# Performance work log

Measured on AMD Instinct MI355X. Metric: run time of the kernel, lower is better.

## Reference

```python
import jax, jax.numpy as jnp
import numpy as np

N = 100000   # nodes
E = 1600000  # edges (avg degree 16)
DIN = 128
DH = 64


def setup_inputs() -> dict:
    key = jax.random.key(0)
    ks = jax.random.split(key, 6)
    x = jax.random.normal(ks[0], (N, DIN), dtype=jnp.float32)
    edge_index = jax.random.randint(ks[1], (2, E), 0, N, dtype=jnp.int32)
    W1 = jax.random.normal(ks[2], (DIN, DH), dtype=jnp.float32) * (1.0 / np.sqrt(DIN))
    b1 = jnp.zeros((DH,), dtype=jnp.float32)
    W2 = jax.random.normal(ks[3], (DH, DH), dtype=jnp.float32) * (1.0 / np.sqrt(DH))
    b2 = jnp.zeros((DH,), dtype=jnp.float32)
    alpha = jnp.full((DH,), 0.25, dtype=jnp.float32)  # PReLU per-channel slope (torch default 0.25)
    return {"x": x, "edge_index": edge_index, "W1": W1, "b1": b1, "W2": W2, "b2": b2, "alpha": alpha}


def _gcn_layer(h, src, dst, norm, W, b):
    # GCNConv: linear transform, then normalized scatter-add aggregation, then bias
    h = h @ W                                  # [N, dout]
    msg = h[src] * norm[:, None]               # [E+N, dout] gathered + scaled messages
    agg = jax.ops.segment_sum(msg, dst, num_segments=N)
    return agg + b


def reference(x, edge_index, W1, b1, W2, b2, alpha):
    src0, dst0 = edge_index[0], edge_index[1]
    # GCNConv default: add self-loops, symmetric normalization deg^{-1/2} A deg^{-1/2}
    loops = jnp.arange(N, dtype=src0.dtype)
    src = jnp.concatenate([src0, loops])
    dst = jnp.concatenate([dst0, loops])
    ones = jnp.ones(src.shape[0], dtype=x.dtype)
    deg = jax.ops.segment_sum(ones, dst, num_segments=N)
    dinv = jnp.where(deg > 0, jax.lax.rsqrt(deg), 0.0)
    norm = dinv[src] * dinv[dst]               # [E+N]

    prelu = lambda z: jnp.where(z >= 0, z, alpha * z)  # shared per-channel PReLU
    z = prelu(_gcn_layer(x, src, dst, norm, W1, b1))
    z = prelu(_gcn_layer(z, src, dst, norm, W2, b2))
    return z
```

## Files before the change

kernel.cpp:

```cpp
#include <hip/hip_runtime.h>
#include <hip/hip_bf16.h>

#define NN 100000
#define NE 1600000
#define NBUCK 391
#define CAP 5120
#define CHUNK 2048
#define PBLOCKS 782
#define MMBLOCKS 1563

typedef __attribute__((ext_vector_type(8))) short short8;
typedef __attribute__((ext_vector_type(4))) float f32x4;

static __device__ __forceinline__ unsigned short f2bf(float f) {
    unsigned u = __float_as_uint(f);
    unsigned r = (u + 0x7fffu + ((u >> 16) & 1u)) >> 16;
    return (unsigned short)r;
}
static __device__ __forceinline__ float bf_lo(unsigned u) {
    return __uint_as_float(u << 16);
}
static __device__ __forceinline__ float bf_hi(unsigned u) {
    return __uint_as_float(u & 0xffff0000u);
}
static __device__ __forceinline__ void acc8(float* acc, uint4 v, float nm) {
    acc[0] += bf_lo(v.x) * nm; acc[1] += bf_hi(v.x) * nm;
    acc[2] += bf_lo(v.y) * nm; acc[3] += bf_hi(v.y) * nm;
    acc[4] += bf_lo(v.z) * nm; acc[5] += bf_hi(v.z) * nm;
    acc[6] += bf_lo(v.w) * nm; acc[7] += bf_hi(v.w) * nm;
}

__global__ __launch_bounds__(256) void k_fat(const int* __restrict__ ei,
                                             int* __restrict__ bcur,
                                             unsigned* __restrict__ ebuf,
                                             const float* __restrict__ x,
                                             const float* __restrict__ W1,
                                             unsigned short* __restrict__ hout) {
    __shared__ __attribute__((aligned(16))) unsigned char smem[17408];
    int tid = threadIdx.x;
    if (blockIdx.x < PBLOCKS) {
        int* lh = (int*)smem;
        int* lbase = lh + NBUCK;
        int e0 = blockIdx.x * CHUNK;
        for (int i = tid; i < NBUCK; i += 256) lh[i] = 0;
        __syncthreads();
        #pragma unroll
        for (int k = 0; k < CHUNK; k += 256) {
            int e = e0 + k + tid;
            if (e < NE) atomicAdd(&lh[ei[NE + e] >> 8], 1);
        }
        __syncthreads();
        for (int i = tid; i < NBUCK; i += 256) {
            int c = lh[i];
            lbase[i] = c ? atomicAdd(&bcur[i], c) : 0;
            lh[i] = 0;
        }
        __syncthreads();
        #pragma unroll
        for (int k = 0; k < CHUNK; k += 256) {
            int e = e0 + k + tid;
            if (e < NE) {
                int d = ei[NE + e];
                int s = ei[e];
                int b = d >> 8;
                int r = atomicAdd(&lh[b], 1);
                int pos = lbase[b] + r;
                if (pos < CAP)
                    ebuf[(long)b * CAP + pos] = ((unsigned)s << 8) | (unsigned)(d & 255);
            }
        }
    } else {
        constexpr int K = 128, KP = K + 8;
        unsigned short* Wt = (unsigned short*)smem;
        for (int idx = tid; idx < K * 64; idx += 256) {
            int k = idx >> 6, n = idx & 63;
            Wt[n * KP + k] = f2bf(W1[idx]);
        }
        __syncthreads();
        int wave = tid >> 6, lane = tid & 63;
        int m = lane & 15, q = lane >> 4;
        int n0 = (blockIdx.x - PBLOCKS) * 64 + wave * 16;
        f32x4 acc[4] = {{0.f,0.f,0.f,0.f},{0.f,0.f,0.f,0.f},{0.f,0.f,0.f,0.f},{0.f,0.f,0.f,0.f}};
        int row = n0 + m;
        int rowc = row < NN ? row : NN - 1;
        const float* xr = x + (long)rowc * K;
        #pragma unroll
        for (int kk = 0; kk < K / 32; ++kk) {
            const float4* p = (const float4*)(xr + kk * 32 + q * 8);
            float4 v0 = p[0], v1 = p[1];
            float xv[8] = {v0.x, v0.y, v0.z, v0.w, v1.x, v1.y, v1.z, v1.w};
            short8 afrag;
            #pragma unroll
            for (int i2 = 0; i2 < 8; ++i2) afrag[i2] = (short)f2bf(xv[i2]);
            #pragma unroll
            for (int nt = 0; nt < 4; ++nt) {
                const short8* bp = (const short8*)&Wt[(nt * 16 + m) * KP + kk * 32 + q * 8];
                acc[nt] = __builtin_amdgcn_mfma_f32_16x16x32_bf16(afrag, *bp, acc[nt], 0, 0, 0);
            }
        }
        #pragma unroll
        for (int reg = 0; reg < 4; ++reg) {
            int node = n0 + q * 4 + reg;
            if (node < NN) {
                #pragma unroll
                for (int nt = 0; nt < 4; ++nt)
                    hout[(long)node * 64 + nt * 16 + m] = f2bf(acc[nt][reg]);
            }
        }
    }
}

__global__ __launch_bounds__(256) void k_build(const int* __restrict__ bcur,
                                               const unsigned* __restrict__ ebuf,
                                               unsigned* __restrict__ rowinfo,
                                               float* __restrict__ dinv,
                                               int* __restrict__ esrc) {
    __shared__ int cnt[256];
    __shared__ int wsum[4];
    int tid = threadIdx.x;
    int base = blockIdx.x * CAP;
    int nedge = bcur[blockIdx.x];
    if (nedge > CAP) nedge = CAP;
    cnt[tid] = 0;
    __syncthreads();
    for (int j = tid; j < nedge; j += 256)
        atomicAdd(&cnt[ebuf[base + j] & 255u], 1);
    __syncthreads();
    int v = cnt[tid];
    int lane = tid & 63;
    int incl = v;
    #pragma unroll
    for (int off = 1; off < 64; off <<= 1) {
        int t = __shfl_up(incl, off, 64);
        if (lane >= off) incl += t;
    }
    if (lane == 63) wsum[tid >> 6] = incl;
    __syncthreads();
    if (tid == 0) {
        int a = 0;
        #pragma unroll
        for (int w = 0; w < 4; ++w) { int t = wsum[w]; wsum[w] = a; a += t; }
    }
    __syncthreads();
    int ex = incl - v + wsum[tid >> 6];
    int node = blockIdx.x * 256 + tid;
    if (node < NN) {
        rowinfo[node] = ((unsigned)(base + ex) << 11) | (unsigned)v;
        dinv[node] = rsqrtf((float)(v + 1));
    }
    cnt[tid] = base + ex;
    __syncthreads();
    for (int j = tid; j < nedge; j += 256) {
        unsigned p = ebuf[base + j];
        int pos = atomicAdd(&cnt[p & 255u], 1);
        esrc[pos] = (int)(p >> 8);
    }
}

__global__ __launch_bounds__(256) void k_mm64(const unsigned short* __restrict__ in_,
                                              const float* __restrict__ W,
                                              unsigned short* __restrict__ hout) {
    constexpr int K = 64, KP = K + 8;
    __shared__ unsigned short Wt[64 * KP];
    int tid = threadIdx.x;
    for (int idx = tid; idx < K * 64; idx += 256) {
        int k = idx >> 6, n = idx & 63;
        Wt[n * KP + k] = f2bf(W[idx]);
    }
    __syncthreads();
    int wave = tid >> 6, lane = tid & 63;
    int m = lane & 15, q = lane >> 4;
    int n0 = blockIdx.x * 64 + wave * 16;
    f32x4 acc[4] = {{0.f,0.f,0.f,0.f},{0.f,0.f,0.f,0.f},{0.f,0.f,0.f,0.f},{0.f,0.f,0.f,0.f}};
    int row = n0 + m;
    int rowc = row < NN ? row : NN - 1;
    const unsigned short* xr = in_ + (long)rowc * K;
    #pragma unroll
    for (int kk = 0; kk < K / 32; ++kk) {
        short8 afrag = *(const short8*)(xr + kk * 32 + q * 8);
        #pragma unroll
        for (int nt = 0; nt < 4; ++nt) {
            const short8* bp = (const short8*)&Wt[(nt * 16 + m) * KP + kk * 32 + q * 8];
            acc[nt] = __builtin_amdgcn_mfma_f32_16x16x32_bf16(afrag, *bp, acc[nt], 0, 0, 0);
        }
    }
    #pragma unroll
    for (int reg = 0; reg < 4; ++reg) {
        int node = n0 + q * 4 + reg;
        if (node < NN) {
            #pragma unroll
            for (int nt = 0; nt < 4; ++nt)
                hout[(long)node * 64 + nt * 16 + m] = f2bf(acc[nt][reg]);
        }
    }
}

template <bool OUT_BF16>
__global__ __launch_bounds__(256) void k_agg(const unsigned* __restrict__ rowinfo,
                                             const int* __restrict__ esrc,
                                             const unsigned short* __restrict__ h,
                                             const float* __restrict__ dinv,
                                             const float* __restrict__ bias,
                                             const float* __restrict__ alpha,
                                             void* __restrict__ out_) {
    int sl = threadIdx.x & 7;
    int node = blockIdx.x * 32 + (threadIdx.x >> 3);
    if (node >= NN) return;
    unsigned u = rowinfo[node];
    int start = (int)(u >> 11);
    int cnt = (int)(u & 2047u);
    float dn = dinv[node];
    const unsigned short* hc = h + sl * 8;

    float acc[8];
    {
        uint4 hw = *(const uint4*)(hc + (long)node * 64);
        float d2 = dn * dn;
        acc[0] = bf_lo(hw.x) * d2; acc[1] = bf_hi(hw.x) * d2;
        acc[2] = bf_lo(hw.y) * d2; acc[3] = bf_hi(hw.y) * d2;
        acc[4] = bf_lo(hw.z) * d2; acc[5] = bf_hi(hw.z) * d2;
        acc[6] = bf_lo(hw.w) * d2; acc[7] = bf_hi(hw.w) * d2;
    }

    int i = 0;
    for (; i + 8 <= cnt; i += 8) {
        int s0 = esrc[start + i];
        int s1 = esrc[start + i + 1];
        int s2 = esrc[start + i + 2];
        int s3 = esrc[start + i + 3];
        int s4 = esrc[start + i + 4];
        int s5 = esrc[start + i + 5];
        int s6 = esrc[start + i + 6];
        int s7 = esrc[start + i + 7];
        float n0 = dinv[s0] * dn, n1 = dinv[s1] * dn;
        float n2 = dinv[s2] * dn, n3 = dinv[s3] * dn;
        float n4 = dinv[s4] * dn, n5 = dinv[s5] * dn;
        float n6 = dinv[s6] * dn, n7 = dinv[s7] * dn;
        uint4 w0 = *(const uint4*)(hc + (long)s0 * 64);
        uint4 w1 = *(const uint4*)(hc + (long)s1 * 64);
        uint4 w2 = *(const uint4*)(hc + (long)s2 * 64);
        uint4 w3 = *(const uint4*)(hc + (long)s3 * 64);
        uint4 w4 = *(const uint4*)(hc + (long)s4 * 64);
        uint4 w5 = *(const uint4*)(hc + (long)s5 * 64);
        uint4 w6 = *(const uint4*)(hc + (long)s6 * 64);
        uint4 w7 = *(const uint4*)(hc + (long)s7 * 64);
        acc8(acc, w0, n0); acc8(acc, w1, n1); acc8(acc, w2, n2); acc8(acc, w3, n3);
        acc8(acc, w4, n4); acc8(acc, w5, n5); acc8(acc, w6, n6); acc8(acc, w7, n7);
    }
    if (i + 4 <= cnt) {
        int s0 = esrc[start + i];
        int s1 = esrc[start + i + 1];
        int s2 = esrc[start + i + 2];
        int s3 = esrc[start + i + 3];
        float n0 = dinv[s0] * dn, n1 = dinv[s1] * dn;
        float n2 = dinv[s2] * dn, n3 = dinv[s3] * dn;
        uint4 w0 = *(const uint4*)(hc + (long)s0 * 64);
        uint4 w1 = *(const uint4*)(hc + (long)s1 * 64);
        uint4 w2 = *(const uint4*)(hc + (long)s2 * 64);
        uint4 w3 = *(const uint4*)(hc + (long)s3 * 64);
        acc8(acc, w0, n0); acc8(acc, w1, n1); acc8(acc, w2, n2); acc8(acc, w3, n3);
        i += 4;
    }
    for (; i < cnt; ++i) {
        int s0 = esrc[start + i];
        float n0 = dinv[s0] * dn;
        uint4 w0 = *(const uint4*)(hc + (long)s0 * 64);
        acc8(acc, w0, n0);
    }

    float4 blo = *(const float4*)(bias + sl * 8);
    float4 bhi = *(const float4*)(bias + sl * 8 + 4);
    float4 alo = *(const float4*)(alpha + sl * 8);
    float4 ahi = *(const float4*)(alpha + sl * 8 + 4);
    float bb[8] = {blo.x, blo.y, blo.z, blo.w, bhi.x, bhi.y, bhi.z, bhi.w};
    float aa[8] = {alo.x, alo.y, alo.z, alo.w, ahi.x, ahi.y, ahi.z, ahi.w};
    #pragma unroll
    for (int j = 0; j < 8; ++j) {
        float v = acc[j] + bb[j];
        acc[j] = v >= 0.f ? v : aa[j] * v;
    }

    if (OUT_BF16) {
        uint4 pk;
        pk.x = (unsigned)f2bf(acc[0]) | ((unsigned)f2bf(acc[1]) << 16);
        pk.y = (unsigned)f2bf(acc[2]) | ((unsigned)f2bf(acc[3]) << 16);
        pk.z = (unsigned)f2bf(acc[4]) | ((unsigned)f2bf(acc[5]) << 16);
        pk.w = (unsigned)f2bf(acc[6]) | ((unsigned)f2bf(acc[7]) << 16);
        *(uint4*)((unsigned short*)out_ + (long)node * 64 + sl * 8) = pk;
    } else {
        float* op = (float*)out_ + (long)node * 64 + sl * 8;
        *(float4*)op = make_float4(acc[0], acc[1], acc[2], acc[3]);
        *(float4*)(op + 4) = make_float4(acc[4], acc[5], acc[6], acc[7]);
    }
}

extern "C" void kernel_launch(void* const* d_in, const int* in_sizes, int n_in,
                              void* d_out, int out_size, void* d_ws, size_t ws_size,
                              hipStream_t stream) {
    const float* x     = (const float*)d_in[0];
    const int*   ei    = (const int*)d_in[1];
    const float* W1    = (const float*)d_in[2];
    const float* b1    = (const float*)d_in[3];
    const float* W2    = (const float*)d_in[4];
    const float* b2    = (const float*)d_in[5];
    const float* alpha = (const float*)d_in[6];
    float* out = (float*)d_out;

    char* ws = (char*)d_ws;
    float*    dinv      = (float*)(ws);
    unsigned* rowinfo   = (unsigned*)(ws + 400384);
    int*      bcur      = (int*)(ws + 800768);
    int*      esrc      = (int*)(ws + 802816);
    unsigned short* hbf = (unsigned short*)(ws + 8810496);
    unsigned* ebuf      = (unsigned*)(ws + 21610496);
    unsigned short* aggbf = (unsigned short*)(ws + 21610496);

    (void)hipMemsetAsync(bcur, 0, NBUCK * sizeof(int), stream);
    k_fat<<<PBLOCKS + MMBLOCKS, 256, 0, stream>>>(ei, bcur, ebuf, x, W1, hbf);
    k_build<<<NBUCK, 256, 0, stream>>>(bcur, ebuf, rowinfo, dinv, esrc);

    k_agg<true><<<(NN + 31) / 32, 256, 0, stream>>>(rowinfo, esrc, hbf, dinv, b1, alpha, aggbf);
    k_mm64<<<(NN + 63) / 64, 256, 0, stream>>>(aggbf, W2, hbf);
    k_agg<false><<<(NN + 31) / 32, 256, 0, stream>>>(rowinfo, esrc, hbf, dinv, b2, alpha, out);
}
```

Measured before the change: 243.9 us.

## Fuse layer-1 aggregation with layer-2 matmul and single-pass edge bucketing

Merges the first aggregation kernel with the W2 MFMA matmul. Each block stages its 32 aggregated rows in shared memory and multiplies them by W2 there, so the bf16 intermediate no longer makes a round trip through global memory and one launch is removed. The bucketing pass now reads the edge list once and keeps bucket, rank and packed value in registers instead of re-reading and re-counting. It also shortens the aggregation unroll from 8 to 4, drops the node bounds checks (relying on NN being divisible by 32), and leaves two of four waves idle during the matmul.

```diff
diff --git a/kernel.cpp b/kernel.cpp
--- a/kernel.cpp
+++ b/kernel.cpp
@@ -28,6 +28,33 @@
     acc[2] += bf_lo(v.y) * nm; acc[3] += bf_hi(v.y) * nm;
     acc[4] += bf_lo(v.z) * nm; acc[5] += bf_hi(v.z) * nm;
     acc[6] += bf_lo(v.w) * nm; acc[7] += bf_hi(v.w) * nm;
+}
+
+static __device__ __forceinline__ void agg_loop(const unsigned short* hc,
+                                                const int* __restrict__ esrc,
+                                                const float* __restrict__ dinv,
+                                                int start, int cnt, float dn,
+                                                float* acc) {
+    int i = 0;
+    for (; i + 4 <= cnt; i += 4) {
+        int s0 = esrc[start + i];
+        int s1 = esrc[start + i + 1];
+        int s2 = esrc[start + i + 2];
+        int s3 = esrc[start + i + 3];
+        float n0 = dinv[s0] * dn, n1 = dinv[s1] * dn;
+        float n2 = dinv[s2] * dn, n3 = dinv[s3] * dn;
+        uint4 w0 = *(const uint4*)(hc + (long)s0 * 64);
+        uint4 w1 = *(const uint4*)(hc + (long)s1 * 64);
+        uint4 w2 = *(const uint4*)(hc + (long)s2 * 64);
+        uint4 w3 = *(const uint4*)(hc + (long)s3 * 64);
+        acc8(acc, w0, n0); acc8(acc, w1, n1); acc8(acc, w2, n2); acc8(acc, w3, n3);
+    }
+    for (; i < cnt; ++i) {
+        int s0 = esrc[start + i];
+        float n0 = dinv[s0] * dn;
+        uint4 w0 = *(const uint4*)(hc + (long)s0 * 64);
+        acc8(acc, w0, n0);
+    }
 }
 
 __global__ __launch_bounds__(256) void k_fat(const int* __restrict__ ei,
@@ -44,29 +71,32 @@
         int e0 = blockIdx.x * CHUNK;
         for (int i = tid; i < NBUCK; i += 256) lh[i] = 0;
         __syncthreads();
-        #pragma unroll
-        for (int k = 0; k < CHUNK; k += 256) {
-            int e = e0 + k + tid;
-            if (e < NE) atomicAdd(&lh[ei[NE + e] >> 8], 1);
+        int bs[8]; int rs[8]; unsigned ps[8];
+        #pragma unroll
+        for (int k = 0; k < 8; ++k) {
+            int e = e0 + k * 256 + tid;
+            bs[k] = -1;
+            if (e < NE) {
+                int d = ei[NE + e];
+                int s = ei[e];
+                int b = d >> 8;
+                bs[k] = b;
+                rs[k] = atomicAdd(&lh[b], 1);
+                ps[k] = ((unsigned)s << 8) | (unsigned)(d & 255);
+            }
         }
         __syncthreads();
         for (int i = tid; i < NBUCK; i += 256) {
             int c = lh[i];
             lbase[i] = c ? atomicAdd(&bcur[i], c) : 0;
-            lh[i] = 0;
         }
         __syncthreads();
         #pragma unroll
-        for (int k = 0; k < CHUNK; k += 256) {
-            int e = e0 + k + tid;
-            if (e < NE) {
-                int d = ei[NE + e];
-                int s = ei[e];
-                int b = d >> 8;
-                int r = atomicAdd(&lh[b], 1);
-                int pos = lbase[b] + r;
+        for (int k = 0; k < 8; ++k) {
+            if (bs[k] >= 0) {
+                int pos = lbase[bs[k]] + rs[k];
                 if (pos < CAP)
-                    ebuf[(long)b * CAP + pos] = ((unsigned)s << 8) | (unsigned)(d & 255);
+                    ebuf[(long)bs[k] * CAP + pos] = ps[k];
             }
         }
     } else {
@@ -157,55 +187,24 @@
     }
 }
 
-__global__ __launch_bounds__(256) void k_mm64(const unsigned short* __restrict__ in_,
-                                              const float* __restrict__ W,
-                                              unsigned short* __restrict__ hout) {
-    constexpr int K = 64, KP = K + 8;
-    __shared__ unsigned short Wt[64 * KP];
+__global__ __launch_bounds__(256) void k_aggmm(const unsigned* __restrict__ rowinfo,
+                                               const int* __restrict__ esrc,
+                                               const unsigned short* __restrict__ h,
+                                               const float* __restrict__ dinv,
+                                               const float* __restrict__ bias,
+                                               const float* __restrict__ alpha,
+                                               const float* __restrict__ W2,
+                                               unsigned short* __restrict__ hout2) {
+    __shared__ unsigned short Wt[64 * 72];
+    __shared__ unsigned short aggs[32 * 72];
     int tid = threadIdx.x;
-    for (int idx = tid; idx < K * 64; idx += 256) {
+    for (int idx = tid; idx < 64 * 64; idx += 256) {
         int k = idx >> 6, n = idx & 63;
-        Wt[n * KP + k] = f2bf(W[idx]);
-    }
-    __syncthreads();
-    int wave = tid >> 6, lane = tid & 63;
-    int m = lane & 15, q = lane >> 4;
-    int n0 = blockIdx.x * 64 + wave * 16;
-    f32x4 acc[4] = {{0.f,0.f,0.f,0.f},{0.f,0.f,0.f,0.f},{0.f,0.f,0.f,0.f},{0.f,0.f,0.f,0.f}};
-    int row = n0 + m;
-    int rowc = row < NN ? row : NN - 1;
-    const unsigned short* xr = in_ + (long)rowc * K;
-    #pragma unroll
-    for (int kk = 0; kk < K / 32; ++kk) {
-        short8 afrag = *(const short8*)(xr + kk * 32 + q * 8);
-        #pragma unroll
-        for (int nt = 0; nt < 4; ++nt) {
-            const short8* bp = (const short8*)&Wt[(nt * 16 + m) * KP + kk * 32 + q * 8];
-            acc[nt] = __builtin_amdgcn_mfma_f32_16x16x32_bf16(afrag, *bp, acc[nt], 0, 0, 0);
-        }
-    }
-    #pragma unroll
-    for (int reg = 0; reg < 4; ++reg) {
-        int node = n0 + q * 4 + reg;
-        if (node < NN) {
-            #pragma unroll
-            for (int nt = 0; nt < 4; ++nt)
-                hout[(long)node * 64 + nt * 16 + m] = f2bf(acc[nt][reg]);
-        }
-    }
-}
-
-template <bool OUT_BF16>
-__global__ __launch_bounds__(256) void k_agg(const unsigned* __restrict__ rowinfo,
-                                             const int* __restrict__ esrc,
-                                             const unsigned short* __restrict__ h,
-                                             const float* __restrict__ dinv,
-                                             const float* __restrict__ bias,
-                                             const float* __restrict__ alpha,
-                                             void* __restrict__ out_) {
-    int sl = threadIdx.x & 7;
-    int node = blockIdx.x * 32 + (threadIdx.x >> 3);
-    if (node >= NN) return;
+        Wt[n * 72 + k] = f2bf(W2[idx]);
+    }
+    int sl = tid & 7;
+    int ln = tid >> 3;
+    int node = blockIdx.x * 32 + ln;
     unsigned u = rowinfo[node];
     int start = (int)(u >> 11);
     int cnt = (int)(u & 2047u);
@@ -221,52 +220,7 @@
         acc[4] = bf_lo(hw.z) * d2; acc[5] = bf_hi(hw.z) * d2;
         acc[6] = bf_lo(hw.w) * d2; acc[7] = bf_hi(hw.w) * d2;
     }
-
-    int i = 0;
-    for (; i + 8 <= cnt; i += 8) {
-        int s0 = esrc[start + i];
-        int s1 = esrc[start + i + 1];
-        int s2 = esrc[start + i + 2];
-        int s3 = esrc[start + i + 3];
-        int s4 = esrc[start + i + 4];
-        int s5 = esrc[start + i + 5];
-        int s6 = esrc[start + i + 6];
-        int s7 = esrc[start + i + 7];
-        float n0 = dinv[s0] * dn, n1 = dinv[s1] * dn;
-        float n2 = dinv[s2] * dn, n3 = dinv[s3] * dn;
-        float n4 = dinv[s4] * dn, n5 = dinv[s5] * dn;
-        float n6 = dinv[s6] * dn, n7 = dinv[s7] * dn;
-        uint4 w0 = *(const uint4*)(hc + (long)s0 * 64);
-        uint4 w1 = *(const uint4*)(hc + (long)s1 * 64);
-        uint4 w2 = *(const uint4*)(hc + (long)s2 * 64);
-        uint4 w3 = *(const uint4*)(hc + (long)s3 * 64);
-        uint4 w4 = *(const uint4*)(hc + (long)s4 * 64);
-        uint4 w5 = *(const uint4*)(hc + (long)s5 * 64);
-        uint4 w6 = *(const uint4*)(hc + (long)s6 * 64);
-        uint4 w7 = *(const uint4*)(hc + (long)s7 * 64);
-        acc8(acc, w0, n0); acc8(acc, w1, n1); acc8(acc, w2, n2); acc8(acc, w3, n3);
-        acc8(acc, w4, n4); acc8(acc, w5, n5); acc8(acc, w6, n6); acc8(acc, w7, n7);
-    }
-    if (i + 4 <= cnt) {
-        int s0 = esrc[start + i];
-        int s1 = esrc[start + i + 1];
-        int s2 = esrc[start + i + 2];
-        int s3 = esrc[start + i + 3];
-        float n0 = dinv[s0] * dn, n1 = dinv[s1] * dn;
-        float n2 = dinv[s2] * dn, n3 = dinv[s3] * dn;
-        uint4 w0 = *(const uint4*)(hc + (long)s0 * 64);
-        uint4 w1 = *(const uint4*)(hc + (long)s1 * 64);
-        uint4 w2 = *(const uint4*)(hc + (long)s2 * 64);
-        uint4 w3 = *(const uint4*)(hc + (long)s3 * 64);
-        acc8(acc, w0, n0); acc8(acc, w1, n1); acc8(acc, w2, n2); acc8(acc, w3, n3);
-        i += 4;
-    }
-    for (; i < cnt; ++i) {
-        int s0 = esrc[start + i];
-        float n0 = dinv[s0] * dn;
-        uint4 w0 = *(const uint4*)(hc + (long)s0 * 64);
-        acc8(acc, w0, n0);
-    }
+    agg_loop(hc, esrc, dinv, start, cnt, dn, acc);
 
     float4 blo = *(const float4*)(bias + sl * 8);
     float4 bhi = *(const float4*)(bias + sl * 8 + 4);
@@ -279,19 +233,79 @@
         float v = acc[j] + bb[j];
         acc[j] = v >= 0.f ? v : aa[j] * v;
     }
-
-    if (OUT_BF16) {
-        uint4 pk;
-        pk.x = (unsigned)f2bf(acc[0]) | ((unsigned)f2bf(acc[1]) << 16);
-        pk.y = (unsigned)f2bf(acc[2]) | ((unsigned)f2bf(acc[3]) << 16);
-        pk.z = (unsigned)f2bf(acc[4]) | ((unsigned)f2bf(acc[5]) << 16);
-        pk.w = (unsigned)f2bf(acc[6]) | ((unsigned)f2bf(acc[7]) << 16);
-        *(uint4*)((unsigned short*)out_ + (long)node * 64 + sl * 8) = pk;
-    } else {
-        float* op = (float*)out_ + (long)node * 64 + sl * 8;
-        *(float4*)op = make_float4(acc[0], acc[1], acc[2], acc[3]);
-        *(float4*)(op + 4) = make_float4(acc[4], acc[5], acc[6], acc[7]);
-    }
+    uint4 pk;
+    pk.x = (unsigned)f2bf(acc[0]) | ((unsigned)f2bf(acc[1]) << 16);
+    pk.y = (unsigned)f2bf(acc[2]) | ((unsigned)f2bf(acc[3]) << 16);
+    pk.z = (unsigned)f2bf(acc[4]) | ((unsigned)f2bf(acc[5]) << 16);
+    pk.w = (unsigned)f2bf(acc[6]) | ((unsigned)f2bf(acc[7]) << 16);
+    *(uint4*)&aggs[ln * 72 + sl * 8] = pk;
+    __syncthreads();
+
+    int wave = tid >> 6;
+    if (wave < 2) {
+        int lane = tid & 63;
+        int m = lane & 15, q = lane >> 4;
+        int row = wave * 16 + m;
+        f32x4 c2[4] = {{0.f,0.f,0.f,0.f},{0.f,0.f,0.f,0.f},{0.f,0.f,0.f,0.f},{0.f,0.f,0.f,0.f}};
+        #pragma unroll
+        for (int kk = 0; kk < 2; ++kk) {
+            short8 afrag = *(const short8*)&aggs[row * 72 + kk * 32 + q * 8];
+            #pragma unroll
+            for (int nt = 0; nt < 4; ++nt) {
+                const short8* bp = (const short8*)&Wt[(nt * 16 + m) * 72 + kk * 32 + q * 8];
+                c2[nt] = __builtin_amdgcn_mfma_f32_16x16x32_bf16(afrag, *bp, c2[nt], 0, 0, 0);
+            }
+        }
+        #pragma unroll
+        for (int reg = 0; reg < 4; ++reg) {
+            int nd = blockIdx.x * 32 + wave * 16 + q * 4 + reg;
+            #pragma unroll
+            for (int nt = 0; nt < 4; ++nt)
+                hout2[(long)nd * 64 + nt * 16 + m] = f2bf(c2[nt][reg]);
+        }
+    }
+}
+
+__global__ __launch_bounds__(256) void k_agg2(const unsigned* __restrict__ rowinfo,
+                                              const int* __restrict__ esrc,
+                                              const unsigned short* __restrict__ h,
+                                              const float* __restrict__ dinv,
+                                              const float* __restrict__ bias,
+                                              const float* __restrict__ alpha,
+                                              float* __restrict__ out) {
+    int sl = threadIdx.x & 7;
+    int node = blockIdx.x * 32 + (threadIdx.x >> 3);
+    unsigned u = rowinfo[node];
+    int start = (int)(u >> 11);
+    int cnt = (int)(u & 2047u);
+    float dn = dinv[node];
+    const unsigned short* hc = h + sl * 8;
+
+    float acc[8];
+    {
+        uint4 hw = *(const uint4*)(hc + (long)node * 64);
+        float d2 = dn * dn;
+        acc[0] = bf_lo(hw.x) * d2; acc[1] = bf_hi(hw.x) * d2;
+        acc[2] = bf_lo(hw.y) * d2; acc[3] = bf_hi(hw.y) * d2;
+        acc[4] = bf_lo(hw.z) * d2; acc[5] = bf_hi(hw.z) * d2;
+        acc[6] = bf_lo(hw.w) * d2; acc[7] = bf_hi(hw.w) * d2;
+    }
+    agg_loop(hc, esrc, dinv, start, cnt, dn, acc);
+
+    float4 blo = *(const float4*)(bias + sl * 8);
+    float4 bhi = *(const float4*)(bias + sl * 8 + 4);
+    float4 alo = *(const float4*)(alpha + sl * 8);
+    float4 ahi = *(const float4*)(alpha + sl * 8 + 4);
+    float bb[8] = {blo.x, blo.y, blo.z, blo.w, bhi.x, bhi.y, bhi.z, bhi.w};
+    float aa[8] = {alo.x, alo.y, alo.z, alo.w, ahi.x, ahi.y, ahi.z, ahi.w};
+    #pragma unroll
+    for (int j = 0; j < 8; ++j) {
+        float v = acc[j] + bb[j];
+        acc[j] = v >= 0.f ? v : aa[j] * v;
+    }
+    float* op = out + (long)node * 64 + sl * 8;
+    *(float4*)op = make_float4(acc[0], acc[1], acc[2], acc[3]);
+    *(float4*)(op + 4) = make_float4(acc[4], acc[5], acc[6], acc[7]);
 }
 
 extern "C" void kernel_launch(void* const* d_in, const int* in_sizes, int n_in,
@@ -313,13 +327,11 @@
     int*      esrc      = (int*)(ws + 802816);
     unsigned short* hbf = (unsigned short*)(ws + 8810496);
     unsigned* ebuf      = (unsigned*)(ws + 21610496);
-    unsigned short* aggbf = (unsigned short*)(ws + 21610496);
+    unsigned short* hbf2 = (unsigned short*)(ws + 21610496);
 
     (void)hipMemsetAsync(bcur, 0, NBUCK * sizeof(int), stream);
     k_fat<<<PBLOCKS + MMBLOCKS, 256, 0, stream>>>(ei, bcur, ebuf, x, W1, hbf);
     k_build<<<NBUCK, 256, 0, stream>>>(bcur, ebuf, rowinfo, dinv, esrc);
-
-    k_agg<true><<<(NN + 31) / 32, 256, 0, stream>>>(rowinfo, esrc, hbf, dinv, b1, alpha, aggbf);
-    k_mm64<<<(NN + 63) / 64, 256, 0, stream>>>(aggbf, W2, hbf);
-    k_agg<false><<<(NN + 31) / 32, 256, 0, stream>>>(rowinfo, esrc, hbf, dinv, b2, alpha, out);
-}
+    k_aggmm<<<NN / 32, 256, 0, stream>>>(rowinfo, esrc, hbf, dinv, b1, alpha, W2, hbf2);
+    k_agg2<<<NN / 32, 256, 0, stream>>>(rowinfo, esrc, hbf2, dinv, b2, alpha, out);
+}
```

Measured after the change: 226.0 us. -7.3%, faster.
